# Kernel optimization log

Hardware: AMD Instinct MI355X
Metric: run time of the kernel (lower is better)

Reference implementation:

```python
import jax, jax.numpy as jnp
import numpy as np

NUM_HEADS = 16
EMB_DIM = 1024
HEAD_DIM = EMB_DIM // NUM_HEADS


def setup_inputs() -> dict:
    key = jax.random.key(0)
    k1, k2, k3, k4 = jax.random.split(key, 4)
    B, S = 2, 2048
    X = jax.random.normal(k1, (B, S, EMB_DIM), dtype=jnp.float32)
    # torch Linear(in, out, bias=False): y = x @ W.T ; store as [in, out]
    Wq = jax.random.normal(k2, (EMB_DIM, EMB_DIM), dtype=jnp.float32) * (EMB_DIM ** -0.5)
    Wk = jax.random.normal(k3, (EMB_DIM, HEAD_DIM), dtype=jnp.float32) * (EMB_DIM ** -0.5)
    Wv = jax.random.normal(k4, (EMB_DIM, HEAD_DIM), dtype=jnp.float32) * (EMB_DIM ** -0.5)
    return {"X": X, "Wq": Wq, "Wk": Wk, "Wv": Wv}


def reference(X, Wq, Wk, Wv):
    B, S, E = X.shape
    H, D = NUM_HEADS, HEAD_DIM
    q = (X @ Wq).reshape(B, S, H, D).transpose(0, 2, 1, 3)  # [B,H,S,D]
    k = X @ Wk  # [B,S,D] shared K head
    v = X @ Wv  # [B,S,D] shared V head
    scores = jnp.einsum('bhsd,btd->bhst', q, k) / jnp.sqrt(jnp.float32(D))
    causal = jnp.tril(jnp.ones((S, S), dtype=bool))
    scores = jnp.where(causal, scores, -jnp.inf)
    probs = jax.nn.softmax(scores, axis=-1)  # [B,H,S,S]
    out = jnp.einsum('bhst,btd->bhsd', probs, v)  # [B,H,S,D]
    return out.transpose(0, 2, 1, 3).reshape(B, S, E)
```

## Files before the change

### kernel.cpp

```cpp
#include <hip/hip_runtime.h>
#include <stdint.h>

#define NH   16
#define EMB  1024
#define HD   64
#define BSZ  2
#define SEQ  2048
#define NROW (BSZ * SEQ)

typedef __attribute__((ext_vector_type(8))) short bf16x8;
typedef __attribute__((ext_vector_type(4))) float f32x4;

__device__ __forceinline__ uint16_t f2bf(float f) {
    union { float f; uint32_t i; } v; v.f = f;
    uint32_t r = v.i + 0x7FFFu + ((v.i >> 16) & 1u);
    return (uint16_t)(r >> 16);
}
__device__ __forceinline__ uint32_t pack2(float a, float b) {
    return (uint32_t)f2bf(a) | ((uint32_t)f2bf(b) << 16);
}
__device__ __forceinline__ uint32_t cvtpk(float a, float b) {
    uint32_t r;
    asm("v_cvt_pk_bf16_f32 %0, %1, %2" : "=v"(r) : "v"(a), "v"(b));
    return r;
}

__device__ __forceinline__ void gl2lds16(const uint16_t* g, uint16_t* l) {
    __builtin_amdgcn_global_load_lds(
        static_cast<const uint32_t*>(static_cast<const void*>(g)),
        static_cast<uint32_t*>(static_cast<void*>(l)), 16, 0, 0);
}

__global__ __launch_bounds__(256) void prep(
    const float* __restrict__ X, uint16_t* __restrict__ Xbf,
    const float* __restrict__ Wq, const float* __restrict__ Wk,
    const float* __restrict__ Wv, uint16_t* __restrict__ Wqt,
    uint16_t* __restrict__ Wkt, uint16_t* __restrict__ Wvt)
{
    __shared__ uint16_t T[64][72];
    const int tid = threadIdx.x;
    if (blockIdx.x < 2048) {
        size_t idx = ((size_t)blockIdx.x * 256 + tid) * 8;
        float4 a = *(const float4*)&X[idx];
        float4 b = *(const float4*)&X[idx + 4];
        *(uint4*)&Xbf[idx] = make_uint4(pack2(a.x, a.y), pack2(a.z, a.w),
                                        pack2(b.x, b.y), pack2(b.z, b.w));
        return;
    }
    const int id = blockIdx.x - 2048;
    const float* W; uint16_t* Wt; int k0, n0, ldw;
    if (id < 256)      { W = Wq; Wt = Wqt; k0 = (id >> 4) * 64; n0 = (id & 15) * 64; ldw = EMB; }
    else if (id < 272) { W = Wk; Wt = Wkt; k0 = (id - 256) * 64; n0 = 0; ldw = HD; }
    else               { W = Wv; Wt = Wvt; k0 = (id - 272) * 64; n0 = 0; ldw = HD; }

    const int r = tid >> 2, c4 = (tid & 3) * 16;
#pragma unroll
    for (int i = 0; i < 4; ++i) {
        float4 wv = *(const float4*)&W[(size_t)(k0 + r) * ldw + n0 + c4 + 4 * i];
        T[r][c4 + 4 * i + 0] = f2bf(wv.x); T[r][c4 + 4 * i + 1] = f2bf(wv.y);
        T[r][c4 + 4 * i + 2] = f2bf(wv.z); T[r][c4 + 4 * i + 3] = f2bf(wv.w);
    }
    __syncthreads();
    const int n = tid >> 2, kk = (tid & 3) * 16;
    uint32_t o[8];
#pragma unroll
    for (int i = 0; i < 8; ++i)
        o[i] = (uint32_t)T[kk + 2 * i][n] | ((uint32_t)T[kk + 2 * i + 1][n] << 16);
    uint16_t* dst = &Wt[(size_t)(n0 + n) * EMB + k0 + kk];
    *(uint4*)dst       = make_uint4(o[0], o[1], o[2], o[3]);
    *(uint4*)(dst + 8) = make_uint4(o[4], o[5], o[6], o[7]);
}

__global__ __launch_bounds__(256) void qkv_gemm_mfma5(
    const uint16_t* __restrict__ Xbf, const uint16_t* __restrict__ Wqt,
    const uint16_t* __restrict__ Wkt, const uint16_t* __restrict__ Wvt,
    float* __restrict__ Qout, uint16_t* __restrict__ Kbf,
    uint16_t* __restrict__ Vtbf)
{
    const int tid  = threadIdx.x;
    const int w    = tid >> 6, lane = tid & 63;
    const int l    = lane & 15, quad = lane >> 4;
    const int wm   = w & 1, wn = w >> 1;
    const int nt   = blockIdx.x;
    const int m0   = blockIdx.y * 64;

    __shared__ uint16_t As[2][64 * 64];
    __shared__ uint16_t Bs[2][128 * 64];

    const uint16_t* gA[2]; uint32_t ldsA[2];
    const uint16_t* gB[4]; uint32_t ldsB[4];
#pragma unroll
    for (int i = 0; i < 2; ++i) {
        int G = (w * 2 + i) * 64 + lane;
        int r = G >> 3, cg = (G & 7) ^ (r & 7);
        gA[i] = &Xbf[(size_t)(m0 + r) * EMB + cg * 8];
        ldsA[i] = (w * 2 + i) * 512;
    }
#pragma unroll
    for (int i = 0; i < 4; ++i) {
        int G = (w * 4 + i) * 64 + lane;
        int r = G >> 3, cg = (G & 7) ^ (r & 7);
        const uint16_t* bs;
        if (nt < 8)      bs = &Wqt[(size_t)(nt * 128 + r) * EMB + cg * 8];
        else if (r < 64) bs = &Wkt[(size_t)r * EMB + cg * 8];
        else             bs = &Wvt[(size_t)(r - 64) * EMB + cg * 8];
        gB[i] = bs;
        ldsB[i] = (w * 4 + i) * 512;
    }

    uint32_t offA[2][2], offB[4][2];
#pragma unroll
    for (int i = 0; i < 2; ++i)
#pragma unroll
        for (int kh = 0; kh < 2; ++kh) {
            int row = 32 * wm + 16 * i + l;
            offA[i][kh] = row * 64 + (((kh * 4 + quad) ^ (row & 7)) * 8);
        }
#pragma unroll
    for (int j = 0; j < 4; ++j)
#pragma unroll
        for (int kh = 0; kh < 2; ++kh) {
            int row = 64 * wn + 16 * j + l;
            offB[j][kh] = row * 64 + (((kh * 4 + quad) ^ (row & 7)) * 8);
        }

    f32x4 acc[2][4] = {};

#pragma unroll
    for (int i = 0; i < 2; ++i) { gl2lds16(gA[i], &As[0][ldsA[i]]); gA[i] += 64; }
#pragma unroll
    for (int i = 0; i < 4; ++i) { gl2lds16(gB[i], &Bs[0][ldsB[i]]); gB[i] += 64; }
    __syncthreads();

    for (int ks = 0; ks < 16; ++ks) {
        const int cur = ks & 1, nxt = cur ^ 1;
        if (ks < 15) {
#pragma unroll
            for (int i = 0; i < 2; ++i) { gl2lds16(gA[i], &As[nxt][ldsA[i]]); gA[i] += 64; }
#pragma unroll
            for (int i = 0; i < 4; ++i) { gl2lds16(gB[i], &Bs[nxt][ldsB[i]]); gB[i] += 64; }
        }
#pragma unroll
        for (int kh = 0; kh < 2; ++kh) {
            bf16x8 af[2], bfr[4];
#pragma unroll
            for (int i = 0; i < 2; ++i) af[i] = *(const bf16x8*)&As[cur][offA[i][kh]];
#pragma unroll
            for (int j = 0; j < 4; ++j) bfr[j] = *(const bf16x8*)&Bs[cur][offB[j][kh]];
#pragma unroll
            for (int i = 0; i < 2; ++i)
#pragma unroll
                for (int j = 0; j < 4; ++j)
                    acc[i][j] = __builtin_amdgcn_mfma_f32_16x16x32_bf16(
                        af[i], bfr[j], acc[i][j], 0, 0, 0);
        }
        __syncthreads();
    }

    if (nt < 8) {
#pragma unroll
        for (int i = 0; i < 2; ++i)
#pragma unroll
            for (int j = 0; j < 4; ++j)
#pragma unroll
                for (int r = 0; r < 4; ++r)
                    Qout[(size_t)(m0 + 32 * wm + 16 * i + 4 * quad + r) * EMB
                         + nt * 128 + 64 * wn + 16 * j + l] = acc[i][j][r];
    } else if (wn == 0) {
#pragma unroll
        for (int i = 0; i < 2; ++i)
#pragma unroll
            for (int j = 0; j < 4; ++j)
#pragma unroll
                for (int r = 0; r < 4; ++r)
                    Kbf[(size_t)(m0 + 32 * wm + 16 * i + 4 * quad + r) * HD
                        + 16 * j + l] = f2bf(acc[i][j][r]);
    } else {
#pragma unroll
        for (int i = 0; i < 2; ++i)
#pragma unroll
            for (int j = 0; j < 4; ++j)
#pragma unroll
                for (int r = 0; r < 4; ++r)
                    Vtbf[(size_t)(16 * j + l) * NROW
                         + m0 + 32 * wm + 16 * i + 4 * quad + r] = f2bf(acc[i][j][r]);
    }
}

__global__ __launch_bounds__(256) void mqa_attn(
    const uint16_t* __restrict__ Kbf, const uint16_t* __restrict__ Vtbf,
    float* __restrict__ Out)
{
    const int tid  = threadIdx.x;
    const int w    = tid >> 6;
    const int lane = tid & 63;
    const int l    = lane & 15;
    const int quad = lane >> 4;
    const int i  = blockIdx.x;
    const int h  = blockIdx.y, b = blockIdx.z;
    const int qt0 = 31 - i, qt1 = i;
    const int q00 = qt0 * 64, q01 = qt1 * 64;

    __shared__ __align__(16) uint16_t KV[2][2][64][72];
    __shared__ __align__(16) uint16_t Ps[2][64][72];

    const float C = 0.125f * 1.4426950408889634f;
    const int sr = tid >> 2, sc = (tid & 3) * 16;

#pragma unroll
    for (int t = 0; t < 2; ++t) {
        const int q0t = t ? q01 : q00;
        const float* src = &Out[(size_t)(b * SEQ + q0t + sr) * EMB + h * HD + sc];
        float4 f0 = *(const float4*)(src + 0);
        float4 f1 = *(const float4*)(src + 4);
        float4 f2 = *(const float4*)(src + 8);
        float4 f3 = *(const float4*)(src + 12);
        *(uint4*)&Ps[t][sr][sc] =
            make_uint4(pack2(f0.x * C, f0.y * C), pack2(f0.z * C, f0.w * C),
                       pack2(f1.x * C, f1.y * C), pack2(f1.z * C, f1.w * C));
        *(uint4*)&Ps[t][sr][sc + 8] =
            make_uint4(pack2(f2.x * C, f2.y * C), pack2(f2.z * C, f2.w * C),
                       pack2(f3.x * C, f3.y * C), pack2(f3.z * C, f3.w * C));
    }

    uint4 kg0, kg1, vg0, vg1;
    {
        const uint4* ks = (const uint4*)&Kbf[(size_t)(b * SEQ + sr) * HD + sc];
        kg0 = ks[0]; kg1 = ks[1];
        const uint4* vs = (const uint4*)&Vtbf[(size_t)sr * NROW + b * SEQ + sc];
        vg0 = vs[0]; vg1 = vs[1];
    }
    *(uint4*)&KV[0][0][sr][sc]     = kg0;
    *(uint4*)&KV[0][0][sr][sc + 8] = kg1;
    *(uint4*)&KV[0][1][sr][sc]     = vg0;
    *(uint4*)&KV[0][1][sr][sc + 8] = vg1;
    {
        const uint4* ks = (const uint4*)&Kbf[(size_t)(b * SEQ + 64 + sr) * HD + sc];
        kg0 = ks[0]; kg1 = ks[1];
        const uint4* vs = (const uint4*)&Vtbf[(size_t)sr * NROW + b * SEQ + 64 + sc];
        vg0 = vs[0]; vg1 = vs[1];
    }
    __syncthreads();

    bf16x8 qf[2][2];
#pragma unroll
    for (int t = 0; t < 2; ++t) {
        qf[t][0] = *(const bf16x8*)&Ps[t][16 * w + l][quad * 8];
        qf[t][1] = *(const bf16x8*)&Ps[t][16 * w + l][32 + quad * 8];
    }

    bf16x8 ones;
#pragma unroll
    for (int j = 0; j < 8; ++j) ones[j] = (short)0x3F80;

    f32x4 accO[2][4] = {};
    f32x4 accSum[2] = {};
    const int qi_l = 16 * w + l;

    auto body = [&](int kb, bool DO1, bool M0, bool M1) __attribute__((always_inline)) {
        const int cur = kb & 1, nxt = cur ^ 1;

        bf16x8 ka[4][2];
#pragma unroll
        for (int ts = 0; ts < 4; ++ts) {
            ka[ts][0] = *(const bf16x8*)&KV[cur][0][16 * ts + l][quad * 8];
            ka[ts][1] = *(const bf16x8*)&KV[cur][0][16 * ts + l][32 + quad * 8];
        }

        if (kb < qt0) {
            *(uint4*)&KV[nxt][0][sr][sc]     = kg0;
            *(uint4*)&KV[nxt][0][sr][sc + 8] = kg1;
            *(uint4*)&KV[nxt][1][sr][sc]     = vg0;
            *(uint4*)&KV[nxt][1][sr][sc + 8] = vg1;
            if (kb + 1 < qt0) {
                const int k0n = (kb + 2) * 64;
                const uint4* ks = (const uint4*)&Kbf[(size_t)(b * SEQ + k0n + sr) * HD + sc];
                kg0 = ks[0]; kg1 = ks[1];
                const uint4* vs = (const uint4*)&Vtbf[(size_t)sr * NROW + b * SEQ + k0n + sc];
                vg0 = vs[0]; vg1 = vs[1];
            }
        }

        f32x4 accS0[4] = {}, accS1[4] = {};
        __builtin_amdgcn_s_setprio(1);
#pragma unroll
        for (int ts = 0; ts < 4; ++ts) {
            accS0[ts] = __builtin_amdgcn_mfma_f32_16x16x32_bf16(ka[ts][0], qf[0][0], accS0[ts], 0, 0, 0);
            accS0[ts] = __builtin_amdgcn_mfma_f32_16x16x32_bf16(ka[ts][1], qf[0][1], accS0[ts], 0, 0, 0);
        }
        if (DO1) {
#pragma unroll
            for (int ts = 0; ts < 4; ++ts) {
                accS1[ts] = __builtin_amdgcn_mfma_f32_16x16x32_bf16(ka[ts][0], qf[1][0], accS1[ts], 0, 0, 0);
                accS1[ts] = __builtin_amdgcn_mfma_f32_16x16x32_bf16(ka[ts][1], qf[1][1], accS1[ts], 0, 0, 0);
            }
        }
        __builtin_amdgcn_s_setprio(0);

        {
            float pv[16];
#pragma unroll
            for (int ts = 0; ts < 4; ++ts)
#pragma unroll
                for (int r = 0; r < 4; ++r)
                    pv[4 * ts + r] = exp2f(accS0[ts][r]);
            if (M0) {
#pragma unroll
                for (int ts = 0; ts < 4; ++ts)
#pragma unroll
                    for (int r = 0; r < 4; ++r)
                        if ((16 * ts + 4 * quad + r) > qi_l) pv[4 * ts + r] = 0.f;
            }
#pragma unroll
            for (int ts = 0; ts < 4; ++ts)
                *(uint2*)&Ps[0][16 * w + l][16 * ts + 4 * quad] =
                    make_uint2(cvtpk(pv[4 * ts + 0], pv[4 * ts + 1]),
                               cvtpk(pv[4 * ts + 2], pv[4 * ts + 3]));
        }
        if (DO1) {
            float pv[16];
#pragma unroll
            for (int ts = 0; ts < 4; ++ts)
#pragma unroll
                for (int r = 0; r < 4; ++r)
                    pv[4 * ts + r] = exp2f(accS1[ts][r]);
            if (M1) {
#pragma unroll
                for (int ts = 0; ts < 4; ++ts)
#pragma unroll
                    for (int r = 0; r < 4; ++r)
                        if ((16 * ts + 4 * quad + r) > qi_l) pv[4 * ts + r] = 0.f;
            }
#pragma unroll
            for (int ts = 0; ts < 4; ++ts)
                *(uint2*)&Ps[1][16 * w + l][16 * ts + 4 * quad] =
                    make_uint2(cvtpk(pv[4 * ts + 0], pv[4 * ts + 1]),
                               cvtpk(pv[4 * ts + 2], pv[4 * ts + 3]));
        }

        bf16x8 vb[4][2];
#pragma unroll
        for (int tn = 0; tn < 4; ++tn) {
            vb[tn][0] = *(const bf16x8*)&KV[cur][1][16 * tn + l][quad * 8];
            vb[tn][1] = *(const bf16x8*)&KV[cur][1][16 * tn + l][32 + quad * 8];
        }

        bf16x8 pa00 = *(const bf16x8*)&Ps[0][16 * w + l][quad * 8];
        bf16x8 pa01 = *(const bf16x8*)&Ps[0][16 * w + l][32 + quad * 8];
        __builtin_amdgcn_s_setprio(1);
#pragma unroll
        for (int tn = 0; tn < 4; ++tn) {
            accO[0][tn] = __builtin_amdgcn_mfma_f32_16x16x32_bf16(pa00, vb[tn][0], accO[0][tn], 0, 0, 0);
            accO[0][tn] = __builtin_amdgcn_mfma_f32_16x16x32_bf16(pa01, vb[tn][1], accO[0][tn], 0, 0, 0);
        }
        accSum[0] = __builtin_amdgcn_mfma_f32_16x16x32_bf16(pa00, ones, accSum[0], 0, 0, 0);
        accSum[0] = __builtin_amdgcn_mfma_f32_16x16x32_bf16(pa01, ones, accSum[0], 0, 0, 0);
        if (DO1) {
            bf16x8 pa10 = *(const bf16x8*)&Ps[1][16 * w + l][quad * 8];
            bf16x8 pa11 = *(const bf16x8*)&Ps[1][16 * w + l][32 + quad * 8];
#pragma unroll
            for (int tn = 0; tn < 4; ++tn) {
                accO[1][tn] = __builtin_amdgcn_mfma_f32_16x16x32_bf16(pa10, vb[tn][0], accO[1][tn], 0, 0, 0);
                accO[1][tn] = __builtin_amdgcn_mfma_f32_16x16x32_bf16(pa11, vb[tn][1], accO[1][tn], 0, 0, 0);
            }
            accSum[1] = __builtin_amdgcn_mfma_f32_16x16x32_bf16(pa10, ones, accSum[1], 0, 0, 0);
            accSum[1] = __builtin_amdgcn_mfma_f32_16x16x32_bf16(pa11, ones, accSum[1], 0, 0, 0);
        }
        __builtin_amdgcn_s_setprio(0);

        __syncthreads();
    };

    for (int kb = 0; kb < qt1; ++kb) body(kb, true,  false, false);
    body(qt1, true,  false, true);
    for (int kb = qt1 + 1; kb < qt0; ++kb) body(kb, false, false, false);
    body(qt0, false, true,  false);

#pragma unroll
    for (int t = 0; t < 2; ++t) {
        const int q0t = t ? q01 : q00;
#pragma unroll
        for (int r = 0; r < 4; ++r) {
            float invr = 1.0f / accSum[t][r];
            const int row = q0t + 16 * w + 4 * quad + r;
#pragma unroll
            for (int tn = 0; tn < 4; ++tn)
                Out[(size_t)(b * SEQ + row) * EMB + h * HD + 16 * tn + l] =
                    accO[t][tn][r] * invr;
        }
    }
}

__global__ __launch_bounds__(256) void qkv_gemm_vec(
    const float* __restrict__ X,  const float* __restrict__ Wq,
    const float* __restrict__ Wk, const float* __restrict__ Wv,
    float* __restrict__ Qout, uint16_t* __restrict__ Kbf,
    uint16_t* __restrict__ Vtbf)
{
    const int tid = threadIdx.x;
    const int tx = tid & 15, ty = tid >> 4;
    const int bx = blockIdx.x;
    const int m0 = blockIdx.y * 64;

    const float* W; int ldw, n0;
    if (bx < 16)       { W = Wq; ldw = EMB; n0 = bx * 64; }
    else if (bx == 16) { W = Wk; ldw = HD;  n0 = 0; }
    else               { W = Wv; ldw = HD;  n0 = 0; }

    __shared__ float sA[64][17];
    __shared__ float sB[16][64];

    float acc[4][4] = {};
    const int arow = tid >> 2, acol = (tid & 3) * 4;
    const int brow = tid >> 4, bcol = (tid & 15) * 4;

    for (int k0 = 0; k0 < EMB; k0 += 16) {
        float4 fa = *(const float4*)&X[(size_t)(m0 + arow) * EMB + k0 + acol];
        float4 fb = *(const float4*)&W[(size_t)(k0 + brow) * ldw + n0 + bcol];
        sA[arow][acol + 0] = fa.x; sA[arow][acol + 1] = fa.y;
        sA[arow][acol + 2] = fa.z; sA[arow][acol + 3] = fa.w;
        sB[brow][bcol + 0] = fb.x; sB[brow][bcol + 1] = fb.y;
        sB[brow][bcol + 2] = fb.z; sB[brow][bcol + 3] = fb.w;
        __syncthreads();
#pragma unroll
        for (int kk = 0; kk < 16; ++kk) {
            float a0 = sA[4 * ty + 0][kk];
            float a1 = sA[4 * ty + 1][kk];
            float a2 = sA[4 * ty + 2][kk];
            float a3 = sA[4 * ty + 3][kk];
            float4 bq = *(const float4*)&sB[kk][4 * tx];
            acc[0][0] += a0 * bq.x; acc[0][1] += a0 * bq.y; acc[0][2] += a0 * bq.z; acc[0][3] += a0 * bq.w;
            acc[1][0] += a1 * bq.x; acc[1][1] += a1 * bq.y; acc[1][2] += a1 * bq.z; acc[1][3] += a1 * bq.w;
            acc[2][0] += a2 * bq.x; acc[2][1] += a2 * bq.y; acc[2][2] += a2 * bq.z; acc[2][3] += a2 * bq.w;
            acc[3][0] += a3 * bq.x; acc[3][1] += a3 * bq.y; acc[3][2] += a3 * bq.z; acc[3][3] += a3 * bq.w;
        }
        __syncthreads();
    }

    if (bx < 16) {
#pragma unroll
        for (int i = 0; i < 4; ++i)
            *(float4*)&Qout[(size_t)(m0 + 4 * ty + i) * EMB + n0 + 4 * tx] =
                make_float4(acc[i][0], acc[i][1], acc[i][2], acc[i][3]);
    } else if (bx == 16) {
#pragma unroll
        for (int i = 0; i < 4; ++i) {
            ushort4 u; u.x = f2bf(acc[i][0]); u.y = f2bf(acc[i][1]);
            u.z = f2bf(acc[i][2]); u.w = f2bf(acc[i][3]);
            *(ushort4*)&Kbf[(size_t)(m0 + 4 * ty + i) * HD + 4 * tx] = u;
        }
    } else {
#pragma unroll
        for (int j = 0; j < 4; ++j) {
            ushort4 u; u.x = f2bf(acc[0][j]); u.y = f2bf(acc[1][j]);
            u.z = f2bf(acc[2][j]); u.w = f2bf(acc[3][j]);
            *(ushort4*)&Vtbf[(size_t)(4 * tx + j) * NROW + m0 + 4 * ty] = u;
        }
    }
}

extern "C" void kernel_launch(void* const* d_in, const int* in_sizes, int n_in,
                              void* d_out, int out_size, void* d_ws, size_t ws_size,
                              hipStream_t stream) {
    const float* X  = (const float*)d_in[0];
    const float* Wq = (const float*)d_in[1];
    const float* Wk = (const float*)d_in[2];
    const float* Wv = (const float*)d_in[3];
    float* OutP = (float*)d_out;

    char* ws = (char*)d_ws;
    const size_t MB = 1024 * 1024;
    uint16_t* Xbf  = (uint16_t*)(ws);
    uint16_t* Wqt  = (uint16_t*)(ws + 8 * MB);
    uint16_t* Wkt  = (uint16_t*)(ws + 10 * MB);
    uint16_t* Wvt  = (uint16_t*)(ws + 10 * MB + 256 * 1024);
    uint16_t* Kbf  = (uint16_t*)(ws + 10 * MB + 512 * 1024);
    uint16_t* Vtbf = (uint16_t*)(ws + 11 * MB);

    if (ws_size >= 12 * MB) {
        prep<<<2336, 256, 0, stream>>>(X, Xbf, Wq, Wk, Wv, Wqt, Wkt, Wvt);
        qkv_gemm_mfma5<<<dim3(9, 64), 256, 0, stream>>>(Xbf, Wqt, Wkt, Wvt,
                                                        OutP, Kbf, Vtbf);
        mqa_attn<<<dim3(16, NH, BSZ), 256, 0, stream>>>(Kbf, Vtbf, OutP);
    } else {
        uint16_t* KbfS  = (uint16_t*)d_ws;
        uint16_t* VtbfS = KbfS + (size_t)NROW * HD;
        qkv_gemm_vec<<<dim3(18, 64), 256, 0, stream>>>(X, Wq, Wk, Wv, OutP, KbfS, VtbfS);
        mqa_attn<<<dim3(16, NH, BSZ), 256, 0, stream>>>(KbfS, VtbfS, OutP);
    }
}
```

Before: 142.7 us.

## Keep P in registers via permuted K rows and read V directly from global

New measurement: 162.8 us. +14.1%, slower.

```diff
diff --git a/kernel.cpp b/kernel.cpp
--- a/kernel.cpp
+++ b/kernel.cpp
@@ -201,11 +201,12 @@
     const int qt0 = 31 - i, qt1 = i;
     const int q00 = qt0 * 64, q01 = qt1 * 64;
 
-    __shared__ __align__(16) uint16_t KV[2][2][64][72];
+    __shared__ __align__(16) uint16_t Ks[2][64][72];
     __shared__ __align__(16) uint16_t Ps[2][64][72];
 
     const float C = 0.125f * 1.4426950408889634f;
     const int sr = tid >> 2, sc = (tid & 3) * 16;
+    const int prow = (sr & 32) + ((sr >> 2) & 3) * 8 + ((sr & 16) >> 2) + (sr & 3);
 
 #pragma unroll
     for (int t = 0; t < 2; ++t) {
@@ -223,22 +224,16 @@
                        pack2(f3.x * C, f3.y * C), pack2(f3.z * C, f3.w * C));
     }
 
-    uint4 kg0, kg1, vg0, vg1;
+    uint4 kg0, kg1;
     {
-        const uint4* ks = (const uint4*)&Kbf[(size_t)(b * SEQ + sr) * HD + sc];
+        const uint4* ks = (const uint4*)&Kbf[(size_t)(b * SEQ + prow) * HD + sc];
         kg0 = ks[0]; kg1 = ks[1];
-        const uint4* vs = (const uint4*)&Vtbf[(size_t)sr * NROW + b * SEQ + sc];
-        vg0 = vs[0]; vg1 = vs[1];
-    }
-    *(uint4*)&KV[0][0][sr][sc]     = kg0;
-    *(uint4*)&KV[0][0][sr][sc + 8] = kg1;
-    *(uint4*)&KV[0][1][sr][sc]     = vg0;
-    *(uint4*)&KV[0][1][sr][sc + 8] = vg1;
+    }
+    *(uint4*)&Ks[0][sr][sc]     = kg0;
+    *(uint4*)&Ks[0][sr][sc + 8] = kg1;
     {
-        const uint4* ks = (const uint4*)&Kbf[(size_t)(b * SEQ + 64 + sr) * HD + sc];
+        const uint4* ks = (const uint4*)&Kbf[(size_t)(b * SEQ + 64 + prow) * HD + sc];
         kg0 = ks[0]; kg1 = ks[1];
-        const uint4* vs = (const uint4*)&Vtbf[(size_t)sr * NROW + b * SEQ + 64 + sc];
-        vg0 = vs[0]; vg1 = vs[1];
     }
     __syncthreads();
 
@@ -257,32 +252,37 @@
     f32x4 accSum[2] = {};
     const int qi_l = 16 * w + l;
 
+    const uint16_t* vbase = &Vtbf[(size_t)l * NROW + b * SEQ + 8 * quad];
+
     auto body = [&](int kb, bool DO1, bool M0, bool M1) __attribute__((always_inline)) {
         const int cur = kb & 1, nxt = cur ^ 1;
 
+        bf16x8 vb[4][2];
+#pragma unroll
+        for (int tn = 0; tn < 4; ++tn)
+#pragma unroll
+            for (int kh = 0; kh < 2; ++kh)
+                vb[tn][kh] = *(const bf16x8*)(vbase + (size_t)(16 * tn) * NROW
+                                              + kb * 64 + 32 * kh);
+
         bf16x8 ka[4][2];
 #pragma unroll
         for (int ts = 0; ts < 4; ++ts) {
-            ka[ts][0] = *(const bf16x8*)&KV[cur][0][16 * ts + l][quad * 8];
-            ka[ts][1] = *(const bf16x8*)&KV[cur][0][16 * ts + l][32 + quad * 8];
+            ka[ts][0] = *(const bf16x8*)&Ks[cur][16 * ts + l][quad * 8];
+            ka[ts][1] = *(const bf16x8*)&Ks[cur][16 * ts + l][32 + quad * 8];
         }
 
         if (kb < qt0) {
-            *(uint4*)&KV[nxt][0][sr][sc]     = kg0;
-            *(uint4*)&KV[nxt][0][sr][sc + 8] = kg1;
-            *(uint4*)&KV[nxt][1][sr][sc]     = vg0;
-            *(uint4*)&KV[nxt][1][sr][sc + 8] = vg1;
+            *(uint4*)&Ks[nxt][sr][sc]     = kg0;
+            *(uint4*)&Ks[nxt][sr][sc + 8] = kg1;
             if (kb + 1 < qt0) {
-                const int k0n = (kb + 2) * 64;
-                const uint4* ks = (const uint4*)&Kbf[(size_t)(b * SEQ + k0n + sr) * HD + sc];
+                const uint4* ks = (const uint4*)
+                    &Kbf[(size_t)(b * SEQ + (kb + 2) * 64 + prow) * HD + sc];
                 kg0 = ks[0]; kg1 = ks[1];
-                const uint4* vs = (const uint4*)&Vtbf[(size_t)sr * NROW + b * SEQ + k0n + sc];
-                vg0 = vs[0]; vg1 = vs[1];
             }
         }
 
         f32x4 accS0[4] = {}, accS1[4] = {};
-        __builtin_amdgcn_s_setprio(1);
 #pragma unroll
         for (int ts = 0; ts < 4; ++ts) {
             accS0[ts] = __builtin_amdgcn_mfma_f32_16x16x32_bf16(ka[ts][0], qf[0][0], accS0[ts], 0, 0, 0);
@@ -295,7 +295,6 @@
                 accS1[ts] = __builtin_amdgcn_mfma_f32_16x16x32_bf16(ka[ts][1], qf[1][1], accS1[ts], 0, 0, 0);
             }
         }
-        __builtin_amdgcn_s_setprio(0);
 
         {
             float pv[16];
@@ -309,13 +308,21 @@
                 for (int ts = 0; ts < 4; ++ts)
 #pragma unroll
                     for (int r = 0; r < 4; ++r)
-                        if ((16 * ts + 4 * quad + r) > qi_l) pv[4 * ts + r] = 0.f;
-            }
-#pragma unroll
-            for (int ts = 0; ts < 4; ++ts)
-                *(uint2*)&Ps[0][16 * w + l][16 * ts + 4 * quad] =
-                    make_uint2(cvtpk(pv[4 * ts + 0], pv[4 * ts + 1]),
-                               cvtpk(pv[4 * ts + 2], pv[4 * ts + 3]));
+                        if ((((ts & 2) << 4) + ((ts & 1) << 2) + 8 * quad + r) > qi_l)
+                            pv[4 * ts + r] = 0.f;
+            }
+            union { uint32_t u[4]; bf16x8 v; } A0, A1;
+#pragma unroll
+            for (int j = 0; j < 4; ++j) A0.u[j] = cvtpk(pv[2 * j],     pv[2 * j + 1]);
+#pragma unroll
+            for (int j = 0; j < 4; ++j) A1.u[j] = cvtpk(pv[8 + 2 * j], pv[9 + 2 * j]);
+#pragma unroll
+            for (int tn = 0; tn < 4; ++tn) {
+                accO[0][tn] = __builtin_amdgcn_mfma_f32_16x16x32_bf16(A0.v, vb[tn][0], accO[0][tn], 0, 0, 0);
+                accO[0][tn] = __builtin_amdgcn_mfma_f32_16x16x32_bf16(A1.v, vb[tn][1], accO[0][tn], 0, 0, 0);
+            }
+            accSum[0] = __builtin_amdgcn_mfma_f32_16x16x32_bf16(A0.v, ones, accSum[0], 0, 0, 0);
+            accSum[0] = __builtin_amdgcn_mfma_f32_16x16x32_bf16(A1.v, ones, accSum[0], 0, 0, 0);
         }
         if (DO1) {
             float pv[16];
@@ -329,46 +336,24 @@
                 for (int ts = 0; ts < 4; ++ts)
 #pragma unroll
                     for (int r = 0; r < 4; ++r)
-                        if ((16 * ts + 4 * quad + r) > qi_l) pv[4 * ts + r] = 0.f;
-            }
-#pragma unroll
-            for (int ts = 0; ts < 4; ++ts)
-                *(uint2*)&Ps[1][16 * w + l][16 * ts + 4 * quad] =
-                    make_uint2(cvtpk(pv[4 * ts + 0], pv[4 * ts + 1]),
-                               cvtpk(pv[4 * ts + 2], pv[4 * ts + 3]));
-        }
-
-        bf16x8 vb[4][2];
-#pragma unroll
-        for (int tn = 0; tn < 4; ++tn) {
-            vb[tn][0] = *(const bf16x8*)&KV[cur][1][16 * tn + l][quad * 8];
-            vb[tn][1] = *(const bf16x8*)&KV[cur][1][16 * tn + l][32 + quad * 8];
-        }
-
-        bf16x8 pa00 = *(const bf16x8*)&Ps[0][16 * w + l][quad * 8];
-        bf16x8 pa01 = *(const bf16x8*)&Ps[0][16 * w + l][32 + quad * 8];
-        __builtin_amdgcn_s_setprio(1);
-#pragma unroll
-        for (int tn = 0; tn < 4; ++tn) {
-            accO[0][tn] = __builtin_amdgcn_mfma_f32_16x16x32_bf16(pa00, vb[tn][0], accO[0][tn], 0, 0, 0);
-            accO[0][tn] = __builtin_amdgcn_mfma_f32_16x16x32_bf16(pa01, vb[tn][1], accO[0][tn], 0, 0, 0);
-        }
-        accSum[0] = __builtin_amdgcn_mfma_f32_16x16x32_bf16(pa00, ones, accSum[0], 0, 0, 0);
-        accSum[0] = __builtin_amdgcn_mfma_f32_16x16x32_bf16(pa01, ones, accSum[0], 0, 0, 0);
-        if (DO1) {
-            bf16x8 pa10 = *(const bf16x8*)&Ps[1][16 * w + l][quad * 8];
-            bf16x8 pa11 = *(const bf16x8*)&Ps[1][16 * w + l][32 + quad * 8];
+                        if ((((ts & 2) << 4) + ((ts & 1) << 2) + 8 * quad + r) > qi_l)
+                            pv[4 * ts + r] = 0.f;
+            }
+            union { uint32_t u[4]; bf16x8 v; } A0, A1;
+#pragma unroll
+            for (int j = 0; j < 4; ++j) A0.u[j] = cvtpk(pv[2 * j],     pv[2 * j + 1]);
+#pragma unroll
+            for (int j = 0; j < 4; ++j) A1.u[j] = cvtpk(pv[8 + 2 * j], pv[9 + 2 * j]);
 #pragma unroll
             for (int tn = 0; tn < 4; ++tn) {
-                accO[1][tn] = __builtin_amdgcn_mfma_f32_16x16x32_bf16(pa10, vb[tn][0], accO[1][tn], 0, 0, 0);
-                accO[1][tn] = __builtin_amdgcn_mfma_f32_16x16x32_bf16(pa11, vb[tn][1], accO[1][tn], 0, 0, 0);
-            }
-            accSum[1] = __builtin_amdgcn_mfma_f32_16x16x32_bf16(pa10, ones, accSum[1], 0, 0, 0);
-            accSum[1] = __builtin_amdgcn_mfma_f32_16x16x32_bf16(pa11, ones, accSum[1], 0, 0, 0);
-        }
-        __builtin_amdgcn_s_setprio(0);
-
-        __syncthreads();
+                accO[1][tn] = __builtin_amdgcn_mfma_f32_16x16x32_bf16(A0.v, vb[tn][0], accO[1][tn], 0, 0, 0);
+                accO[1][tn] = __builtin_amdgcn_mfma_f32_16x16x32_bf16(A1.v, vb[tn][1], accO[1][tn], 0, 0, 0);
+            }
+            accSum[1] = __builtin_amdgcn_mfma_f32_16x16x32_bf16(A0.v, ones, accSum[1], 0, 0, 0);
+            accSum[1] = __builtin_amdgcn_mfma_f32_16x16x32_bf16(A1.v, ones, accSum[1], 0, 0, 0);
+        }
+
+        if (kb < qt0) __syncthreads();
     };
 
     for (int kb = 0; kb < qt1; ++kb) body(kb, true,  false, false);
```
